# Kernel tuning notes

Measured on AMD Instinct MI355X. Metric: run time of the kernel, lower is better.

## Reference

```python
import jax, jax.numpy as jnp
import numpy as np

B, T, E, H = 8, 2048, 1024, 64

def setup_inputs() -> dict:
    key = jax.random.key(0)
    k1, k2, k3, k4 = jax.random.split(key, 4)
    x = jax.random.normal(k1, (B, T, E), dtype=jnp.float32)
    # Linear(E, H, bias=False) weights stored as [E, H] (x @ W)
    s = 1.0 / np.sqrt(E)
    Wk = jax.random.normal(k2, (E, H), dtype=jnp.float32) * s
    Wq = jax.random.normal(k3, (E, H), dtype=jnp.float32) * s
    Wv = jax.random.normal(k4, (E, H), dtype=jnp.float32) * s
    return {"x": x, "Wk": Wk, "Wq": Wq, "Wv": Wv}

def reference(x, Wk, Wq, Wv):
    _, t, e = x.shape
    k = jnp.einsum('bte,eh->bth', x, Wk)
    q = jnp.einsum('bte,eh->bth', x, Wq)
    v = jnp.einsum('bte,eh->bth', x, Wv)
    # NOTE: original scales by E**-0.5 (embedding dim), not head_size**-0.5
    wei = jnp.einsum('bqh,bkh->bqk', q, k) * (e ** -0.5)
    causal = jnp.tril(jnp.ones((t, t), dtype=bool))
    wei = jnp.where(causal, wei, -jnp.inf)
    wei = jax.nn.softmax(wei, axis=-1)
    out = jnp.einsum('bqk,bkh->bqh', wei, v)
    return out
```

## Files before the change

### kernel.cpp

```cpp
#include <hip/hip_runtime.h>

typedef unsigned short u16;
typedef unsigned int u32;
typedef __bf16 bf16x8 __attribute__((ext_vector_type(8)));
typedef __bf16 bf16x4 __attribute__((ext_vector_type(4)));
typedef float f32x4 __attribute__((ext_vector_type(4)));

constexpr int Bn = 8, Tn = 2048, En = 1024, Hn = 64;
constexpr int Mrows = Bn * Tn;
constexpr float CEXP = 0.03125f * 1.4426950408889634f;

__device__ __forceinline__ u16 f2bf(float f) {
  u32 u = __float_as_uint(f);
  return (u16)((u + 0x7fffu + ((u >> 16) & 1u)) >> 16);
}

__global__ __launch_bounds__(256) void wt_kernel(
    const float* __restrict__ Wk, const float* __restrict__ Wq,
    const float* __restrict__ Wv, u16* __restrict__ Wt2) {
  __shared__ float tile[64][68];
  const int mat = blockIdx.x >> 4;
  const int tk = blockIdx.x & 15;
  const float* W = (mat == 0) ? Wk : (mat == 1) ? Wq : Wv;
  const int t = threadIdx.x;
#pragma unroll
  for (int i = 0; i < 4; ++i) {
    const int f = t + i * 256;
    const int el = f >> 4;
    const int h4 = f & 15;
    float4 v = *(const float4*)(W + (size_t)(tk * 64 + el) * Hn + h4 * 4);
    tile[el][h4 * 4 + 0] = v.x;
    tile[el][h4 * 4 + 1] = v.y;
    tile[el][h4 * 4 + 2] = v.z;
    tile[el][h4 * 4 + 3] = v.w;
  }
  __syncthreads();
#pragma unroll
  for (int c2 = 0; c2 < 2; ++c2) {
    const int c = t * 2 + c2;
    const int fi = c >> 6;
    const int l = c & 63;
    const int ht = fi >> 1, kss = fi & 1;
    const int q = l >> 4, l16 = l & 15;
    __align__(16) u16 buf[8];
#pragma unroll
    for (int j = 0; j < 8; ++j)
      buf[j] = f2bf(tile[kss * 32 + q * 8 + j][ht * 16 + l16]);
    u16* dst = Wt2 + ((size_t)(tk * 12 + mat * 4 + ht) * 2 + kss) * 512 + l * 8;
    *(uint4*)dst = *(const uint4*)buf;
  }
}

__global__ __launch_bounds__(256, 1) void qkv_kernel(
    const float* __restrict__ x, const u16* __restrict__ Wt2,
    u16* __restrict__ Kb16, u16* __restrict__ Qb16, u16* __restrict__ Vt16) {
  constexpr int NR = 64, BK = 128, LDK = BK + 8;
  __shared__ u16 xs[2][NR * LDK];
  const int t = threadIdx.x;
  const int w = t >> 6, lane = t & 63;
  const int quad = lane >> 4, l16 = lane & 15;
  const int r0 = blockIdx.x * NR;

  const int srow = t >> 2;
  const int scol = (t & 3) * 32;
  const float* xp = x + (size_t)(r0 + srow) * En + scol;

  const u16* wA = Wt2 + (size_t)lane * 8;

  f32x4 acc[3][4];
#pragma unroll
  for (int i = 0; i < 3; ++i)
#pragma unroll
    for (int rt = 0; rt < 4; ++rt) acc[i][rt] = (f32x4){0.f, 0.f, 0.f, 0.f};

  bf16x8 af[2][12];
  float4 pre[8];

#define LOADP(K0)                                                    \
  do {                                                               \
    _Pragma("unroll") for (int j_ = 0; j_ < 8; ++j_)                 \
        pre[j_] = *(const float4*)(xp + (K0) + j_ * 4);              \
  } while (0)

#define LOADA(P, K0)                                                            \
  do {                                                                          \
    const int tb_ = ((K0) >> 6) * 12;                                           \
    _Pragma("unroll") for (int ks_ = 0; ks_ < 4; ++ks_)                         \
        _Pragma("unroll") for (int i_ = 0; i_ < 3; ++i_) {                      \
      const int frag_ = (tb_ + (ks_ >> 1) * 12 + (3 * w + i_)) * 2 + (ks_ & 1); \
      af[P][ks_ * 3 + i_] = *(const bf16x8*)(wA + (size_t)frag_ * 512);         \
    }                                                                           \
  } while (0)

#define WRITEX(B)                                                    \
  do {                                                               \
    u16* d_ = &xs[B][srow * LDK + scol];                             \
    _Pragma("unroll") for (int j_ = 0; j_ < 4; ++j_) {               \
      bf16x8 pk_;                                                    \
      pk_[0] = (__bf16)pre[2 * j_].x;  pk_[1] = (__bf16)pre[2 * j_].y;  \
      pk_[2] = (__bf16)pre[2 * j_].z;  pk_[3] = (__bf16)pre[2 * j_].w;  \
      pk_[4] = (__bf16)pre[2 * j_ + 1].x; pk_[5] = (__bf16)pre[2 * j_ + 1].y; \
      pk_[6] = (__bf16)pre[2 * j_ + 1].z; pk_[7] = (__bf16)pre[2 * j_ + 1].w; \
      *(bf16x8*)(d_ + j_ * 8) = pk_;                                 \
    }                                                                \
  } while (0)

  LOADP(0);
  LOADA(0, 0);
  WRITEX(0);
  LOADP(BK);

#pragma unroll
  for (int s = 0; s < 8; ++s) {
    __syncthreads();
    if (s < 7) {
      WRITEX((s + 1) & 1);
      if (s < 6) LOADP((s + 2) * BK);
      LOADA((s + 1) & 1, (s + 1) * BK);
    }
    const u16* xb = &xs[s & 1][0];
#pragma unroll
    for (int ks = 0; ks < 4; ++ks) {
#pragma unroll
      for (int rt = 0; rt < 4; ++rt) {
        bf16x8 b = *(const bf16x8*)(xb + (rt * 16 + l16) * LDK + ks * 32 + quad * 8);
#pragma unroll
        for (int i = 0; i < 3; ++i)
          acc[i][rt] = __builtin_amdgcn_mfma_f32_16x16x32_bf16(af[s & 1][ks * 3 + i], b,
                                                               acc[i][rt], 0, 0, 0);
      }
    }
  }
#undef LOADP
#undef LOADA
#undef WRITEX

#pragma unroll
  for (int i = 0; i < 3; ++i) {
    const int mt = 3 * w + i;
    const int mat = mt >> 2, ht = mt & 3;
#pragma unroll
    for (int rt = 0; rt < 4; ++rt) {
      const int row = r0 + rt * 16 + l16;
      f32x4 a = acc[i][rt];
      if (mat < 2) {
        u16* dst = ((mat == 0) ? Kb16 : Qb16) + (size_t)row * Hn + ht * 16 + quad * 4;
        uint2 pk;
        pk.x = (u32)f2bf(a[0]) | ((u32)f2bf(a[1]) << 16);
        pk.y = (u32)f2bf(a[2]) | ((u32)f2bf(a[3]) << 16);
        *(uint2*)dst = pk;
      } else {
        const int bb = row >> 11, tt = row & 2047;
        u16* base = Vt16 + ((size_t)bb * 64) * Tn + tt;
#pragma unroll
        for (int r = 0; r < 4; ++r)
          base[(size_t)(ht * 16 + quad * 4 + r) * Tn] = f2bf(a[r]);
      }
    }
  }
}

__global__ __launch_bounds__(512, 4) void attn_kernel(
    const u16* __restrict__ Qb16, const u16* __restrict__ Kb16,
    const u16* __restrict__ Vt16, float* __restrict__ out) {
  __shared__ __align__(16) char arena[34816];
  __shared__ float l_sh[8][32];

  u16* ptb = (u16*)arena;
  float* osb = (float*)arena;

  const int idx = blockIdx.x;
  const int b = idx & 7;
  const int tq = 63 - (idx >> 3);
  const int w = threadIdx.x >> 6, lane = threadIdx.x & 63;
  const int quad = lane >> 4, l16 = lane & 15;
  const int qbase = tq * 32;
  const int limit = qbase + 32;
  const int ch = ((limit + 255) >> 8) << 5;
  const int lo = w * ch;
  const int hi = min(lo + ch, limit);
  const int qa_abs = qbase + l16;
  const int qb_abs = qbase + 16 + l16;

  const u16* Kp = Kb16 + (size_t)b * Tn * Hn;
  const u16* Vp = Vt16 + (size_t)b * 64 * Tn;

  const u16* qrowA = Qb16 + ((size_t)b * Tn + qa_abs) * Hn + quad * 8;
  const u16* qrowB = qrowA + (size_t)16 * Hn;
  const bf16x8 qa0 = *(const bf16x8*)(qrowA);
  const bf16x8 qa1 = *(const bf16x8*)(qrowA + 32);
  const bf16x8 qb0 = *(const bf16x8*)(qrowB);
  const bf16x8 qb1 = *(const bf16x8*)(qrowB + 32);

  u16* ptw = ptb + (size_t)w * (2 * 16 * 40);

  f32x4 oA0 = {0.f, 0.f, 0.f, 0.f}, oA1 = oA0, oA2 = oA0, oA3 = oA0;
  f32x4 oB0 = oA0, oB1 = oA0, oB2 = oA0, oB3 = oA0;
  f32x4 laccA = oA0, laccB = oA0;

#pragma unroll 2
  for (int kb = lo; kb < hi; kb += 32) {
    const u16* krow0 = Kp + (size_t)(kb + l16) * Hn + quad * 8;
    const u16* krow1 = krow0 + (size_t)16 * Hn;
    const bf16x8 k0lo = *(const bf16x8*)(krow0);
    const bf16x8 k0hi = *(const bf16x8*)(krow0 + 32);
    const bf16x8 k1lo = *(const bf16x8*)(krow1);
    const bf16x8 k1hi = *(const bf16x8*)(krow1 + 32);

    const f32x4 z = {0.f, 0.f, 0.f, 0.f};
    f32x4 s0a = __builtin_amdgcn_mfma_f32_16x16x32_bf16(k0lo, qa0, z, 0, 0, 0);
    s0a = __builtin_amdgcn_mfma_f32_16x16x32_bf16(k0hi, qa1, s0a, 0, 0, 0);
    f32x4 s1a = __builtin_amdgcn_mfma_f32_16x16x32_bf16(k1lo, qa0, z, 0, 0, 0);
    s1a = __builtin_amdgcn_mfma_f32_16x16x32_bf16(k1hi, qa1, s1a, 0, 0, 0);
    f32x4 s0b = __builtin_amdgcn_mfma_f32_16x16x32_bf16(k0lo, qb0, z, 0, 0, 0);
    s0b = __builtin_amdgcn_mfma_f32_16x16x32_bf16(k0hi, qb1, s0b, 0, 0, 0);
    f32x4 s1b = __builtin_amdgcn_mfma_f32_16x16x32_bf16(k1lo, qb0, z, 0, 0, 0);
    s1b = __builtin_amdgcn_mfma_f32_16x16x32_bf16(k1hi, qb1, s1b, 0, 0, 0);

    if (kb + 15 > qbase) {
#pragma unroll
      for (int r = 0; r < 4; ++r)
        if (kb + quad * 4 + r > qa_abs) s0a[r] = -3.0e38f;
    }
    if (kb + 31 > qbase) {
#pragma unroll
      for (int r = 0; r < 4; ++r)
        if (kb + 16 + quad * 4 + r > qa_abs) s1a[r] = -3.0e38f;
    }
    if (kb + 15 > qbase + 16) {
#pragma unroll
      for (int r = 0; r < 4; ++r)
        if (kb + quad * 4 + r > qb_abs) s0b[r] = -3.0e38f;
    }
    if (kb + 31 > qbase + 16) {
#pragma unroll
      for (int r = 0; r < 4; ++r)
        if (kb + 16 + quad * 4 + r > qb_abs) s1b[r] = -3.0e38f;
    }

    f32x4 pa0, pa1, pb0v, pb1v;
#pragma unroll
    for (int r = 0; r < 4; ++r) {
      pa0[r] = __builtin_amdgcn_exp2f(s0a[r] * CEXP);
      pa1[r] = __builtin_amdgcn_exp2f(s1a[r] * CEXP);
      pb0v[r] = __builtin_amdgcn_exp2f(s0b[r] * CEXP);
      pb1v[r] = __builtin_amdgcn_exp2f(s1b[r] * CEXP);
    }
    laccA += pa0;
    laccA += pa1;
    laccB += pb0v;
    laccB += pb1v;

    {
      bf16x4 wa0, wa1, wb0, wb1;
      wa0[0] = (__bf16)pa0[0]; wa0[1] = (__bf16)pa0[1];
      wa0[2] = (__bf16)pa0[2]; wa0[3] = (__bf16)pa0[3];
      wa1[0] = (__bf16)pa1[0]; wa1[1] = (__bf16)pa1[1];
      wa1[2] = (__bf16)pa1[2]; wa1[3] = (__bf16)pa1[3];
      wb0[0] = (__bf16)pb0v[0]; wb0[1] = (__bf16)pb0v[1];
      wb0[2] = (__bf16)pb0v[2]; wb0[3] = (__bf16)pb0v[3];
      wb1[0] = (__bf16)pb1v[0]; wb1[1] = (__bf16)pb1v[1];
      wb1[2] = (__bf16)pb1v[2]; wb1[3] = (__bf16)pb1v[3];
      *(bf16x4*)&ptw[l16 * 40 + quad * 4] = wa0;
      *(bf16x4*)&ptw[l16 * 40 + 16 + quad * 4] = wa1;
      *(bf16x4*)&ptw[640 + l16 * 40 + quad * 4] = wb0;
      *(bf16x4*)&ptw[640 + l16 * 40 + 16 + quad * 4] = wb1;
    }
    const bf16x8 pba = *(const bf16x8*)&ptw[l16 * 40 + quad * 8];
    const bf16x8 pbb = *(const bf16x8*)&ptw[640 + l16 * 40 + quad * 8];

    const u16* vrow = Vp + (size_t)l16 * Tn + kb + quad * 8;
    const bf16x8 v0 = *(const bf16x8*)(vrow);
    const bf16x8 v1 = *(const bf16x8*)(vrow + (size_t)16 * Tn);
    const bf16x8 v2 = *(const bf16x8*)(vrow + (size_t)32 * Tn);
    const bf16x8 v3 = *(const bf16x8*)(vrow + (size_t)48 * Tn);

    oA0 = __builtin_amdgcn_mfma_f32_16x16x32_bf16(v0, pba, oA0, 0, 0, 0);
    oA1 = __builtin_amdgcn_mfma_f32_16x16x32_bf16(v1, pba, oA1, 0, 0, 0);
    oA2 = __builtin_amdgcn_mfma_f32_16x16x32_bf16(v2, pba, oA2, 0, 0, 0);
    oA3 = __builtin_amdgcn_mfma_f32_16x16x32_bf16(v3, pba, oA3, 0, 0, 0);
    oB0 = __builtin_amdgcn_mfma_f32_16x16x32_bf16(v0, pbb, oB0, 0, 0, 0);
    oB1 = __builtin_amdgcn_mfma_f32_16x16x32_bf16(v1, pbb, oB1, 0, 0, 0);
    oB2 = __builtin_amdgcn_mfma_f32_16x16x32_bf16(v2, pbb, oB2, 0, 0, 0);
    oB3 = __builtin_amdgcn_mfma_f32_16x16x32_bf16(v3, pbb, oB3, 0, 0, 0);
  }

  float la = (laccA[0] + laccA[1]) + (laccA[2] + laccA[3]);
  la += __shfl_xor(la, 16);
  la += __shfl_xor(la, 32);
  float lb = (laccB[0] + laccB[1]) + (laccB[2] + laccB[3]);
  lb += __shfl_xor(lb, 16);
  lb += __shfl_xor(lb, 32);
  if (quad == 0) {
    l_sh[w][l16] = la;
    l_sh[w][16 + l16] = lb;
  }
  __syncthreads();

  if (w < 4) {
    float* o0 = osb + ((size_t)w * 32 + l16) * 68;
    *(f32x4*)(o0 + 0 * 16 + quad * 4) = oA0;
    *(f32x4*)(o0 + 1 * 16 + quad * 4) = oA1;
    *(f32x4*)(o0 + 2 * 16 + quad * 4) = oA2;
    *(f32x4*)(o0 + 3 * 16 + quad * 4) = oA3;
    float* o1 = osb + ((size_t)w * 32 + 16 + l16) * 68;
    *(f32x4*)(o1 + 0 * 16 + quad * 4) = oB0;
    *(f32x4*)(o1 + 1 * 16 + quad * 4) = oB1;
    *(f32x4*)(o1 + 2 * 16 + quad * 4) = oB2;
    *(f32x4*)(o1 + 3 * 16 + quad * 4) = oB3;
  }
  __syncthreads();

  const int qq = threadIdx.x >> 4, dq = threadIdx.x & 15;
  f32x4 part = {0.f, 0.f, 0.f, 0.f};
#pragma unroll
  for (int ww = 0; ww < 4; ++ww)
    part += *(const f32x4*)&osb[((size_t)ww * 32 + qq) * 68 + dq * 4];
  __syncthreads();

  if (w >= 4) {
    float* o0 = osb + ((size_t)(w - 4) * 32 + l16) * 68;
    *(f32x4*)(o0 + 0 * 16 + quad * 4) = oA0;
    *(f32x4*)(o0 + 1 * 16 + quad * 4) = oA1;
    *(f32x4*)(o0 + 2 * 16 + quad * 4) = oA2;
    *(f32x4*)(o0 + 3 * 16 + quad * 4) = oA3;
    float* o1 = osb + ((size_t)(w - 4) * 32 + 16 + l16) * 68;
    *(f32x4*)(o1 + 0 * 16 + quad * 4) = oB0;
    *(f32x4*)(o1 + 1 * 16 + quad * 4) = oB1;
    *(f32x4*)(o1 + 2 * 16 + quad * 4) = oB2;
    *(f32x4*)(o1 + 3 * 16 + quad * 4) = oB3;
  }
  __syncthreads();

#pragma unroll
  for (int ww = 0; ww < 4; ++ww)
    part += *(const f32x4*)&osb[((size_t)ww * 32 + qq) * 68 + dq * 4];

  float lg = 0.f;
#pragma unroll
  for (int ww = 0; ww < 8; ++ww) lg += l_sh[ww][qq];
  part *= (1.f / lg);
  *(f32x4*)(out + ((size_t)b * Tn + qbase + qq) * Hn + dq * 4) = part;
}

extern "C" void kernel_launch(void* const* d_in, const int* in_sizes, int n_in,
                              void* d_out, int out_size, void* d_ws, size_t ws_size,
                              hipStream_t stream) {
  const void* x = nullptr;
  const void* Ws[3] = {nullptr, nullptr, nullptr};
  int wj = 0;
  for (int i = 0; i < n_in; ++i) {
    if (in_sizes[i] == Bn * Tn * En) x = d_in[i];
    else if (wj < 3) Ws[wj++] = d_in[i];
  }
  const float* Wk = (const float*)Ws[0];
  const float* Wq = (const float*)Ws[1];
  const float* Wv = (const float*)Ws[2];

  u16* Kb16 = (u16*)d_ws;
  u16* Qb16 = Kb16 + (size_t)Mrows * Hn;
  u16* Vt16 = Qb16 + (size_t)Mrows * Hn;
  u16* Wt2  = Vt16 + (size_t)Mrows * Hn;

  wt_kernel<<<48, 256, 0, stream>>>(Wk, Wq, Wv, Wt2);
  qkv_kernel<<<Mrows / 64, 256, 0, stream>>>((const float*)x, Wt2, Kb16, Qb16, Vt16);
  attn_kernel<<<Bn * (Tn / 32), 512, 0, stream>>>(Qb16, Kb16, Vt16, (float*)d_out);
}
```

Before: 135.8 us.

## Halve QKV projection row tile to 32 and raise occupancy to two blocks

Shrinks the QKV projection block from 64 to 32 rows, doubling the grid to 512 blocks, and raises the launch-bound occupancy hint to 2 blocks per CU. The x staging loads are remapped so each thread reads one float4 per row across four rows, which gives coalesced 512-byte row segments. The __syncthreads is replaced with an inline-asm lgkmcnt wait plus s_barrier, and the weight-fragment prefetch is reordered after the x prefetch. The goal is more parallelism across the 256 CUs and better latency hiding on the memory-bound x read, at the cost of loading the weight fragments twice as often per row.

```diff
diff --git a/kernel.cpp b/kernel.cpp
--- a/kernel.cpp
+++ b/kernel.cpp
@@ -51,35 +51,35 @@
   }
 }
 
-__global__ __launch_bounds__(256, 1) void qkv_kernel(
+__global__ __launch_bounds__(256, 2) void qkv_kernel(
     const float* __restrict__ x, const u16* __restrict__ Wt2,
     u16* __restrict__ Kb16, u16* __restrict__ Qb16, u16* __restrict__ Vt16) {
-  constexpr int NR = 64, BK = 128, LDK = BK + 8;
+  constexpr int NR = 32, BK = 128, LDK = BK + 8;
   __shared__ u16 xs[2][NR * LDK];
   const int t = threadIdx.x;
   const int w = t >> 6, lane = t & 63;
   const int quad = lane >> 4, l16 = lane & 15;
   const int r0 = blockIdx.x * NR;
 
-  const int srow = t >> 2;
-  const int scol = (t & 3) * 32;
+  const int srow = t >> 5;
+  const int scol = (t & 31) * 4;
   const float* xp = x + (size_t)(r0 + srow) * En + scol;
 
   const u16* wA = Wt2 + (size_t)lane * 8;
 
-  f32x4 acc[3][4];
+  f32x4 acc[3][2];
 #pragma unroll
   for (int i = 0; i < 3; ++i)
 #pragma unroll
-    for (int rt = 0; rt < 4; ++rt) acc[i][rt] = (f32x4){0.f, 0.f, 0.f, 0.f};
+    for (int nt = 0; nt < 2; ++nt) acc[i][nt] = (f32x4){0.f, 0.f, 0.f, 0.f};
 
   bf16x8 af[2][12];
-  float4 pre[8];
+  float4 pre[4];
 
 #define LOADP(K0)                                                    \
   do {                                                               \
-    _Pragma("unroll") for (int j_ = 0; j_ < 8; ++j_)                 \
-        pre[j_] = *(const float4*)(xp + (K0) + j_ * 4);              \
+    _Pragma("unroll") for (int j_ = 0; j_ < 4; ++j_)                 \
+        pre[j_] = *(const float4*)(xp + (K0) + j_ * 8 * En);         \
   } while (0)
 
 #define LOADA(P, K0)                                                            \
@@ -96,53 +96,51 @@
   do {                                                               \
     u16* d_ = &xs[B][srow * LDK + scol];                             \
     _Pragma("unroll") for (int j_ = 0; j_ < 4; ++j_) {               \
-      bf16x8 pk_;                                                    \
-      pk_[0] = (__bf16)pre[2 * j_].x;  pk_[1] = (__bf16)pre[2 * j_].y;  \
-      pk_[2] = (__bf16)pre[2 * j_].z;  pk_[3] = (__bf16)pre[2 * j_].w;  \
-      pk_[4] = (__bf16)pre[2 * j_ + 1].x; pk_[5] = (__bf16)pre[2 * j_ + 1].y; \
-      pk_[6] = (__bf16)pre[2 * j_ + 1].z; pk_[7] = (__bf16)pre[2 * j_ + 1].w; \
-      *(bf16x8*)(d_ + j_ * 8) = pk_;                                 \
+      bf16x4 pk_;                                                    \
+      pk_[0] = (__bf16)pre[j_].x; pk_[1] = (__bf16)pre[j_].y;        \
+      pk_[2] = (__bf16)pre[j_].z; pk_[3] = (__bf16)pre[j_].w;        \
+      *(bf16x4*)(d_ + j_ * 8 * LDK) = pk_;                           \
     }                                                                \
   } while (0)
 
+#define BARRIER() asm volatile("s_waitcnt lgkmcnt(0)\ns_barrier" ::: "memory")
+
   LOADP(0);
-  LOADA(0, 0);
   WRITEX(0);
   LOADP(BK);
+  LOADA(0, 0);
 
 #pragma unroll
   for (int s = 0; s < 8; ++s) {
-    __syncthreads();
-    if (s < 7) {
-      WRITEX((s + 1) & 1);
-      if (s < 6) LOADP((s + 2) * BK);
-      LOADA((s + 1) & 1, (s + 1) * BK);
-    }
+    BARRIER();
+    if (s < 7) WRITEX((s + 1) & 1);
+    if (s < 6) LOADP((s + 2) * BK);
+    if (s < 7) LOADA((s + 1) & 1, (s + 1) * BK);
     const u16* xb = &xs[s & 1][0];
 #pragma unroll
     for (int ks = 0; ks < 4; ++ks) {
-#pragma unroll
-      for (int rt = 0; rt < 4; ++rt) {
-        bf16x8 b = *(const bf16x8*)(xb + (rt * 16 + l16) * LDK + ks * 32 + quad * 8);
-#pragma unroll
-        for (int i = 0; i < 3; ++i)
-          acc[i][rt] = __builtin_amdgcn_mfma_f32_16x16x32_bf16(af[s & 1][ks * 3 + i], b,
-                                                               acc[i][rt], 0, 0, 0);
+      bf16x8 b0 = *(const bf16x8*)(xb + l16 * LDK + ks * 32 + quad * 8);
+      bf16x8 b1 = *(const bf16x8*)(xb + (16 + l16) * LDK + ks * 32 + quad * 8);
+#pragma unroll
+      for (int i = 0; i < 3; ++i) {
+        acc[i][0] = __builtin_amdgcn_mfma_f32_16x16x32_bf16(af[s & 1][ks * 3 + i], b0, acc[i][0], 0, 0, 0);
+        acc[i][1] = __builtin_amdgcn_mfma_f32_16x16x32_bf16(af[s & 1][ks * 3 + i], b1, acc[i][1], 0, 0, 0);
       }
     }
   }
 #undef LOADP
 #undef LOADA
 #undef WRITEX
+#undef BARRIER
 
 #pragma unroll
   for (int i = 0; i < 3; ++i) {
     const int mt = 3 * w + i;
     const int mat = mt >> 2, ht = mt & 3;
 #pragma unroll
-    for (int rt = 0; rt < 4; ++rt) {
-      const int row = r0 + rt * 16 + l16;
-      f32x4 a = acc[i][rt];
+    for (int nt = 0; nt < 2; ++nt) {
+      const int row = r0 + nt * 16 + l16;
+      f32x4 a = acc[i][nt];
       if (mat < 2) {
         u16* dst = ((mat == 0) ? Kb16 : Qb16) + (size_t)row * Hn + ht * 16 + quad * 4;
         uint2 pk;
@@ -363,6 +361,6 @@
   u16* Wt2  = Vt16 + (size_t)Mrows * Hn;
 
   wt_kernel<<<48, 256, 0, stream>>>(Wk, Wq, Wv, Wt2);
-  qkv_kernel<<<Mrows / 64, 256, 0, stream>>>((const float*)x, Wt2, Kb16, Qb16, Vt16);
+  qkv_kernel<<<Mrows / 32, 256, 0, stream>>>((const float*)x, Wt2, Kb16, Qb16, Vt16);
   attn_kernel<<<Bn * (Tn / 32), 512, 0, stream>>>(Qb16, Kb16, Vt16, (float*)d_out);
 }
```

Result: no change. 133.3 us (-1.8%).
